# Kernel tuning notes

Measured on AMD Instinct MI355X. Metric: run time of the kernel, lower is better.

## Reference

```python
import jax, jax.numpy as jnp
import numpy as np
from functools import partial


def conv2d(x, w, b, pad):
    # x: [B,C,H,W], w: [O,I,kh,kw]
    out = jax.lax.conv_general_dilated(
        x, w, window_strides=(1, 1), padding=[(pad, pad), (pad, pad)],
        dimension_numbers=("NCHW", "OIHW", "NCHW"))
    return out + b[None, :, None, None]


def maxpool3x3_s1(x):
    return jax.lax.reduce_window(
        x, -jnp.inf, jax.lax.max, (1, 1, 3, 3), (1, 1, 1, 1),
        padding=((0, 0), (0, 0), (1, 1), (1, 1)))


def bilinear_sample(img, y, x):
    # img: [B,C,H,W]; y, x: [B,H,W] float sample coords. Zero outside bounds.
    def one(im, yy, xx):  # im [C,H,W]
        H, W = im.shape[1], im.shape[2]
        y0 = jnp.floor(yy)
        x0 = jnp.floor(xx)
        wy = yy - y0
        wx = xx - x0
        y0i = y0.astype(jnp.int32)
        x0i = x0.astype(jnp.int32)

        def g(yi, xi):
            valid = (yi >= 0) & (yi < H) & (xi >= 0) & (xi < W)
            yc = jnp.clip(yi, 0, H - 1)
            xc = jnp.clip(xi, 0, W - 1)
            return im[:, yc, xc] * valid[None].astype(im.dtype)

        return (g(y0i, x0i) * ((1 - wy) * (1 - wx))[None]
                + g(y0i, x0i + 1) * ((1 - wy) * wx)[None]
                + g(y0i + 1, x0i) * (wy * (1 - wx))[None]
                + g(y0i + 1, x0i + 1) * (wy * wx)[None])

    return jax.vmap(one)(img, y, x)


def deform_conv2d(x, offset, weight, bias, k, pad):
    # torchvision-style: offset [B, 2*k*k, H, W], pairs are (dy, dx) in
    # row-major kernel order. stride=1, dilation=1.
    B, C, H, W = x.shape
    off = offset.reshape(B, k * k, 2, H, W)
    hh = jnp.arange(H, dtype=x.dtype)[None, :, None]  # [1,H,1]
    ww = jnp.arange(W, dtype=x.dtype)[None, None, :]  # [1,1,W]
    out = jnp.zeros((B, weight.shape[0], H, W), x.dtype)
    for t in range(k * k):
        i, j = t // k, t % k
        y = hh + (i - pad) + off[:, t, 0]  # [B,H,W]
        xc = ww + (j - pad) + off[:, t, 1]
        s = bilinear_sample(x, y, xc)      # [B,C,H,W]
        out = out + jnp.einsum("bchw,oc->bohw", s, weight[:, :, i, j])
    return out + bias[None, :, None, None]


def _mk(key, shape, scale=0.05):
    return jax.random.normal(key, shape, dtype=jnp.float32) * scale


def setup_inputs() -> dict:
    key = jax.random.key(0)
    ks = jax.random.split(key, 20)
    C = 512
    Cb = C // 4  # 128
    B, H, W = 8, 64, 64
    return {
        "x": jax.random.normal(ks[0], (B, C, H, W), dtype=jnp.float32),
        "w_b1": _mk(ks[1], (Cb, C, 1, 1)), "b_b1": jnp.zeros((Cb,), jnp.float32),
        "w_b21": _mk(ks[2], (Cb, C, 1, 1)), "b_b21": jnp.zeros((Cb,), jnp.float32),
        "w_off2": _mk(ks[3], (18, Cb, 3, 3), 0.01), "b_off2": jnp.zeros((18,), jnp.float32),
        "w_ddc2": _mk(ks[4], (Cb, Cb, 3, 3)), "b_ddc2": jnp.zeros((Cb,), jnp.float32),
        "w_b31": _mk(ks[5], (Cb, C, 1, 1)), "b_b31": jnp.zeros((Cb,), jnp.float32),
        "w_off3": _mk(ks[6], (50, Cb, 5, 5), 0.01), "b_off3": jnp.zeros((50,), jnp.float32),
        "w_ddc3": _mk(ks[7], (Cb, Cb, 5, 5)), "b_ddc3": jnp.zeros((Cb,), jnp.float32),
        "w_b4": _mk(ks[8], (Cb, C, 1, 1)), "b_b4": jnp.zeros((Cb,), jnp.float32),
        "w_cc": _mk(ks[9], (C, Cb * 4, 1, 1)), "b_cc": jnp.zeros((C,), jnp.float32),
    }


def reference(x, w_b1, b_b1, w_b21, b_b21, w_off2, b_off2, w_ddc2, b_ddc2,
              w_b31, b_b31, w_off3, b_off3, w_ddc3, b_ddc3, w_b4, b_b4,
              w_cc, b_cc):
    b1 = conv2d(x, w_b1, b_b1, 0)

    b2i = conv2d(x, w_b21, b_b21, 0)
    off2 = conv2d(b2i, w_off2, b_off2, 1)
    b2 = deform_conv2d(b2i, off2, w_ddc2, b_ddc2, k=3, pad=1)

    b3i = conv2d(x, w_b31, b_b31, 0)
    off3 = conv2d(b3i, w_off3, b_off3, 2)
    b3 = deform_conv2d(b3i, off3, w_ddc3, b_ddc3, k=5, pad=2)

    b4 = conv2d(maxpool3x3_s1(x), w_b4, b_b4, 0)

    cat = jnp.concatenate([b1, b2, b3, b4], axis=1) * x
    fused = conv2d(cat, w_cc, b_cc, 0)
    return x + jax.nn.sigmoid(fused)
```

## Files before the change

### kernel.cpp

```cpp
#include <hip/hip_runtime.h>
#include <math.h>

#define HW 4096
typedef short short8 __attribute__((ext_vector_type(8)));
typedef float floatx4 __attribute__((ext_vector_type(4)));

#define O_XBT   0ull
#define O_PXB   33554432ull
#define O_CATB  67108864ull
#define O_WPB   100663296ull
#define O_W4B   101056512ull
#define O_WCCB  101187584ull
#define O_WD2T  101711872ull
#define O_WD3T  102006784ull
#define O_WO2T  102825984ull
#define O_WO3T  102973440ull
#define O_T2B   33554432ull
#define O_T3B   41943040ull
#define O_OFF2  50331648ull
#define O_OFF3  52690944ull

__device__ __forceinline__ unsigned short f2b(float f) {
    union { float f; unsigned u; } v; v.f = f;
    unsigned r = v.u + 0x7FFFu + ((v.u >> 16) & 1u);
    return (unsigned short)(r >> 16);
}
__device__ __forceinline__ float lou(unsigned u) {
    union { unsigned u; float f; } v; v.u = u << 16; return v.f;
}
__device__ __forceinline__ float hiu(unsigned u) {
    union { unsigned u; float f; } v; v.u = u & 0xFFFF0000u; return v.f;
}
__device__ __forceinline__ unsigned pk2(float lo, float hi) {
    return (unsigned)f2b(lo) | ((unsigned)f2b(hi) << 16);
}

__global__ __launch_bounds__(256) void k_prepw(
        const float* __restrict__ w1, const float* __restrict__ w21,
        const float* __restrict__ w31, const float* __restrict__ w4,
        const float* __restrict__ wcc, const float* __restrict__ wd2,
        const float* __restrict__ wd3, const float* __restrict__ wo2,
        const float* __restrict__ wo3, unsigned short* __restrict__ ws8) {
    unsigned i = blockIdx.x * 256 + threadIdx.x;
    unsigned short* wpb  = ws8 + (O_WPB  >> 1);
    unsigned short* w4b  = ws8 + (O_W4B  >> 1);
    unsigned short* wccb = ws8 + (O_WCCB >> 1);
    unsigned short* wd2t = ws8 + (O_WD2T >> 1);
    unsigned short* wd3t = ws8 + (O_WD3T >> 1);
    unsigned short* wo2t = ws8 + (O_WO2T >> 1);
    unsigned short* wo3t = ws8 + (O_WO3T >> 1);
    if (i < 196608) {
        int o = i >> 9;
        float v = (o < 128) ? w1[i] : (o < 256) ? w21[i - 65536] : w31[i - 131072];
        wpb[i] = f2b(v);
    } else if (i < 262144) {
        unsigned j = i - 196608; w4b[j] = f2b(w4[j]);
    } else if (i < 524288) {
        unsigned j = i - 262144; wccb[j] = f2b(wcc[j]);
    } else if (i < 671744) {
        unsigned j = i - 524288; int t = j >> 14, o = (j >> 7) & 127, c = j & 127;
        wd2t[j] = f2b(wd2[((o * 128 + c) * 9) + t]);
    } else if (i < 1081344) {
        unsigned j = i - 671744; int t = j >> 14, o = (j >> 7) & 127, c = j & 127;
        wd3t[j] = f2b(wd3[((o * 128 + c) * 25) + t]);
    } else if (i < 1155072) {
        unsigned j = i - 1081344; int t = j >> 13, o = (j >> 7) & 63, c = j & 127;
        wo2t[j] = (o < 18) ? f2b(wo2[((o * 128 + c) * 9) + t]) : 0;
    } else if (i < 1359872) {
        unsigned j = i - 1155072; int t = j >> 13, o = (j >> 7) & 63, c = j & 127;
        wo3t[j] = (o < 50) ? f2b(wo3[((o * 128 + c) * 25) + t]) : 0;
    }
}

__global__ __launch_bounds__(256) void k_xpose(const float* __restrict__ X,
                                               unsigned short* __restrict__ xbT) {
    __shared__ unsigned short t[32][33];
    const int p0 = blockIdx.x * 32, c0 = blockIdx.y * 32, b = blockIdx.z;
    const int tid = threadIdx.x;
    #pragma unroll
    for (int s = 0; s < 4; ++s) {
        int cl = s * 8 + (tid >> 5), pl = tid & 31;
        t[cl][pl] = f2b(X[((size_t)b * 512 + c0 + cl) * HW + p0 + pl]);
    }
    __syncthreads();
    #pragma unroll
    for (int s = 0; s < 4; ++s) {
        int pl = s * 8 + (tid >> 5), cl = tid & 31;
        xbT[((size_t)b * HW + p0 + pl) * 512 + c0 + cl] = t[cl][pl];
    }
}

__global__ __launch_bounds__(256) void k_pool(const unsigned short* __restrict__ xbT,
                                              unsigned short* __restrict__ pxb) {
    unsigned gid = blockIdx.x * 256 + threadIdx.x;
    int b = gid >> 18;
    unsigned rem = gid & 262143;
    int pos = rem >> 6;
    int cg = (rem & 63) * 8;
    int h = pos >> 6, w = pos & 63;
    const unsigned short* img = xbT + (size_t)b * HW * 512;
    float m[8] = {-INFINITY, -INFINITY, -INFINITY, -INFINITY,
                  -INFINITY, -INFINITY, -INFINITY, -INFINITY};
    #pragma unroll
    for (int dy = -1; dy <= 1; ++dy) {
        int hh = h + dy;
        if (hh < 0 || hh >= 64) continue;
        #pragma unroll
        for (int dx = -1; dx <= 1; ++dx) {
            int ww = w + dx;
            if (ww < 0 || ww >= 64) continue;
            uint4 v = *(const uint4*)(img + ((size_t)(hh * 64 + ww)) * 512 + cg);
            unsigned uu[4] = {v.x, v.y, v.z, v.w};
            #pragma unroll
            for (int e = 0; e < 4; ++e) {
                m[2 * e]     = fmaxf(m[2 * e],     lou(uu[e]));
                m[2 * e + 1] = fmaxf(m[2 * e + 1], hiu(uu[e]));
            }
        }
    }
    uint4 o;
    o.x = pk2(m[0], m[1]); o.y = pk2(m[2], m[3]);
    o.z = pk2(m[4], m[5]); o.w = pk2(m[6], m[7]);
    *(uint4*)(pxb + ((size_t)b * HW + pos) * 512 + cg) = o;
}

#define SA(r,c) SM[(r)*40 + (c)]
#define SB(r,c) SM[5120 + (r)*40 + (c)]
#define SC(r,c) SM[(r)*136 + (c)]
__global__ __launch_bounds__(256) void k_gemm(
        const unsigned short* __restrict__ A, const float* __restrict__ bias,
        const unsigned short* __restrict__ Bm,
        unsigned short* __restrict__ dst, int dStride, int dOff) {
    __shared__ unsigned short SM[17408];
    const int tid = threadIdx.x;
    const int n0 = blockIdx.x * 128;
    const int b = blockIdx.z;
    const int wave = tid >> 6, lane = tid & 63, quad = lane >> 4, lr = lane & 15;
    const int m0w = (wave & 1) * 64, n0w = (wave >> 1) * 64;
    const int srow = tid >> 1, skh = (tid & 1) * 16;
    floatx4 acc[4][4] = {};

    for (int k0 = 0; k0 < 512; k0 += 32) {
        const unsigned short* ga = A + (size_t)srow * 512 + k0 + skh;
        uint4 a0 = *(const uint4*)(ga);
        uint4 a1 = *(const uint4*)(ga + 8);
        const unsigned short* gb = Bm + ((size_t)b * HW + n0 + srow) * 512 + k0 + skh;
        uint4 b0 = *(const uint4*)(gb);
        uint4 b1 = *(const uint4*)(gb + 8);
        __syncthreads();
        *(uint4*)&SA(srow, skh) = a0;
        *(uint4*)&SA(srow, skh + 8) = a1;
        *(uint4*)&SB(srow, skh) = b0;
        *(uint4*)&SB(srow, skh + 8) = b1;
        __syncthreads();
        short8 af[4], bf[4];
        #pragma unroll
        for (int i = 0; i < 4; ++i) af[i] = *(short8*)&SA(m0w + i * 16 + lr, quad * 8);
        #pragma unroll
        for (int j = 0; j < 4; ++j) bf[j] = *(short8*)&SB(n0w + j * 16 + lr, quad * 8);
        #pragma unroll
        for (int i = 0; i < 4; ++i)
            #pragma unroll
            for (int j = 0; j < 4; ++j)
                acc[i][j] = __builtin_amdgcn_mfma_f32_16x16x32_bf16(af[i], bf[j], acc[i][j], 0, 0, 0);
    }
    __syncthreads();
    #pragma unroll
    for (int i = 0; i < 4; ++i) {
        float4 bs = *(const float4*)&bias[m0w + i * 16 + quad * 4];
        #pragma unroll
        for (int j = 0; j < 4; ++j) {
            floatx4 v = acc[i][j];
            int pos = n0w + j * 16 + lr;
            int ch = m0w + i * 16 + quad * 4;
            uint2 st;
            st.x = pk2(v[0] + bs.x, v[1] + bs.y);
            st.y = pk2(v[2] + bs.z, v[3] + bs.w);
            *(uint2*)&SC(pos, ch) = st;
        }
    }
    __syncthreads();
    #pragma unroll
    for (int r = 0; r < 8; ++r) {
        int pos = (tid >> 4) + r * 16;
        *(uint4*)&dst[((size_t)b * HW + n0 + pos) * dStride + dOff + (tid & 15) * 8] =
            *(uint4*)&SC(pos, (tid & 15) * 8);
    }
}

template<int KS, int OCH>
__global__ __launch_bounds__(512) void k_offconv2(
        const unsigned short* __restrict__ img,
        const unsigned short* __restrict__ woT,
        const float* __restrict__ bias, float* __restrict__ Out) {
    constexpr int PAD = KS / 2;
    constexpr int TT = KS * KS;
    constexpr int SR = 2 + 2 * PAD;
    constexpr int SC2 = 64 + 2 * PAD;
    constexpr int NE = SR * SC2;
    __shared__ unsigned short slab[NE * 36];
    __shared__ float ctile[64 * 132];
    const int tid = threadIdx.x;
    const int p0 = blockIdx.x * 128, hrow0 = blockIdx.x * 2, b = blockIdx.z;
    const int wave = tid >> 6, lane = tid & 63, quad = lane >> 4, lr = lane & 15;
    const int wm = wave & 1, wn = wave >> 1;
    const unsigned short* ib = img + (size_t)b * HW * 128;
    floatx4 acc[2][2] = {};

    for (int c0 = 0; c0 < 128; c0 += 32) {
        __syncthreads();
        if (tid < NE) {
            int s = tid / SC2, cl = tid % SC2;
            int r = hrow0 - PAD + s, cc = cl - PAD;
            uint4 v0 = {}, v1 = {}, v2 = {}, v3 = {};
            if ((unsigned)r < 64u && (unsigned)cc < 64u) {
                const uint4* g = (const uint4*)(ib + ((size_t)(r * 64 + cc)) * 128 + c0);
                v0 = g[0]; v1 = g[1]; v2 = g[2]; v3 = g[3];
            }
            uint2* d2 = (uint2*)&slab[tid * 36];
            d2[0] = make_uint2(v0.x, v0.y); d2[1] = make_uint2(v0.z, v0.w);
            d2[2] = make_uint2(v1.x, v1.y); d2[3] = make_uint2(v1.z, v1.w);
            d2[4] = make_uint2(v2.x, v2.y); d2[5] = make_uint2(v2.z, v2.w);
            d2[6] = make_uint2(v3.x, v3.y); d2[7] = make_uint2(v3.z, v3.w);
        }
        __syncthreads();
        #pragma unroll
        for (int t = 0; t < TT; ++t) {
            const int ky = t / KS, kx = t % KS;
            short8 af[2], bf[2];
            #pragma unroll
            for (int i = 0; i < 2; ++i)
                af[i] = *(const short8*)&woT[((size_t)t * 64 + wm * 32 + i * 16 + lr) * 128
                                             + c0 + quad * 8];
            #pragma unroll
            for (int j = 0; j < 2; ++j) {
                int p = wn * 32 + j * 16 + lr;
                int e = ((p >> 6) + ky) * SC2 + (p & 63) + kx;
                union { uint2 u[2]; short8 s; } bb;
                const uint2* sp = (const uint2*)&slab[e * 36 + quad * 8];
                bb.u[0] = sp[0]; bb.u[1] = sp[1];
                bf[j] = bb.s;
            }
            #pragma unroll
            for (int i = 0; i < 2; ++i)
                #pragma unroll
                for (int j = 0; j < 2; ++j)
                    acc[i][j] = __builtin_amdgcn_mfma_f32_16x16x32_bf16(af[i], bf[j], acc[i][j], 0, 0, 0);
        }
    }
    __syncthreads();
    #pragma unroll
    for (int i = 0; i < 2; ++i)
        #pragma unroll
        for (int j = 0; j < 2; ++j) {
            floatx4 v = acc[i][j];
            int p = wn * 32 + j * 16 + lr;
            int o = wm * 32 + i * 16 + quad * 4;
            #pragma unroll
            for (int rg = 0; rg < 4; ++rg)
                ctile[(o + rg) * 132 + p] = v[rg];
        }
    __syncthreads();
    {
        int o = tid >> 3, seg = tid & 7;
        if (o < OCH) {
            float bs = bias[o];
            const float* src = &ctile[o * 132 + seg * 16];
            float* dst = &Out[((size_t)b * OCH + o) * HW + p0 + seg * 16];
            #pragma unroll
            for (int q = 0; q < 4; ++q) {
                float4 v = *(const float4*)(src + q * 4);
                v.x += bs; v.y += bs; v.z += bs; v.w += bs;
                *(float4*)(dst + q * 4) = v;
            }
        }
    }
}

#define DC_GATHER(T, DY, DX) do {                                              \
    float fy = (float)(h + (T) / KS - PAD) + (DY);                             \
    float fx = (float)(w + (T) % KS - PAD) + (DX);                             \
    float y0f = floorf(fy), x0f = floorf(fx);                                  \
    float wyv = fy - y0f, wxv = fx - x0f;                                      \
    int y0 = (int)y0f, x0 = (int)x0f;                                          \
    w00 = (1.f - wyv) * (1.f - wxv); w01 = (1.f - wyv) * wxv;                  \
    w10 = wyv * (1.f - wxv);         w11 = wyv * wxv;                          \
    bool yv0 = (unsigned)y0 < 64u, yv1 = (unsigned)(y0 + 1) < 64u;             \
    bool xv0 = (unsigned)x0 < 64u, xv1 = (unsigned)(x0 + 1) < 64u;             \
    long bidx = (long)(y0 * 64 + x0) * 128 + cseg;                             \
    cn0 = z4; cn1 = z4; cn2 = z4; cn3 = z4;                                    \
    cn4 = z4; cn5 = z4; cn6 = z4; cn7 = z4;                                    \
    if (yv0 && xv0) { const uint4* p_ = (const uint4*)(ib + bidx);             \
        cn0 = p_[0]; cn1 = p_[1]; }                                            \
    if (yv0 && xv1) { const uint4* p_ = (const uint4*)(ib + bidx + 128);       \
        cn2 = p_[0]; cn3 = p_[1]; }                                            \
    if (yv1 && xv0) { const uint4* p_ = (const uint4*)(ib + bidx + 8192);      \
        cn4 = p_[0]; cn5 = p_[1]; }                                            \
    if (yv1 && xv1) { const uint4* p_ = (const uint4*)(ib + bidx + 8320);      \
        cn6 = p_[0]; cn7 = p_[1]; }                                            \
} while (0)

#define DC_BLEND(RA, RB, RC, RD, OUT) do {                                     \
    unsigned a_[4] = {RA.x, RA.y, RA.z, RA.w};                                 \
    unsigned b_[4] = {RB.x, RB.y, RB.z, RB.w};                                 \
    unsigned c_[4] = {RC.x, RC.y, RC.z, RC.w};                                 \
    unsigned d_[4] = {RD.x, RD.y, RD.z, RD.w};                                 \
    unsigned r_[4];                                                            \
    _Pragma("unroll")                                                          \
    for (int e_ = 0; e_ < 4; ++e_) {                                           \
        float lo_ = w00 * lou(a_[e_]) + w01 * lou(b_[e_])                      \
                  + w10 * lou(c_[e_]) + w11 * lou(d_[e_]);                     \
        float hi_ = w00 * hiu(a_[e_]) + w01 * hiu(b_[e_])                      \
                  + w10 * hiu(c_[e_]) + w11 * hiu(d_[e_]);                     \
        asm("v_cvt_pk_bf16_f32 %0, %1, %2"                                     \
            : "=v"(r_[e_]) : "v"(lo_), "v"(hi_));                              \
    }                                                                          \
    OUT.x = r_[0]; OUT.y = r_[1]; OUT.z = r_[2]; OUT.w = r_[3];                \
} while (0)

template<int KS>
__global__ __launch_bounds__(256, 4) void k_deform10(
        const unsigned short* __restrict__ img,
        const float* __restrict__ Off,
        const unsigned short* __restrict__ wdT,
        const float* __restrict__ bias,
        unsigned short* __restrict__ catb, int dOff) {
    constexpr int PAD = KS / 2;
    constexpr int TT = KS * KS;
    __shared__ unsigned short sS[2][32][136];
    const int tid = threadIdx.x;
    const int b = blockIdx.x & 7;
    const int tile = (blockIdx.x >> 3) + 16 * blockIdx.z;
    const int p0 = tile * 32;
    const int wave = tid >> 6, lane = tid & 63, quad = lane >> 4, lr = lane & 15;
    const int m0w = wave * 32;
    const int pos = tid >> 3;
    const int cseg = (tid & 7) * 16;
    const int pglob = p0 + pos;
    const int h = pglob >> 6, w = pglob & 63;
    const unsigned short* ib = img + (size_t)b * HW * 128;
    const float* offb = Off + (size_t)b * 2 * TT * HW;
    const uint4 z4 = make_uint4(0u, 0u, 0u, 0u);

    floatx4 acc00 = {}, acc01 = {}, acc10 = {}, acc11 = {};
    uint4 cn0, cn1, cn2, cn3, cn4, cn5, cn6, cn7;
    float w00, w01, w10, w11;
    float noy = 0.f, nox = 0.f;

    {
        float dy0 = offb[pglob];
        float dx0 = offb[HW + pglob];
        DC_GATHER(0, dy0, dx0);
    }
    if (TT > 1) { noy = offb[2 * HW + pglob]; nox = offb[3 * HW + pglob]; }

    for (int t = 0; t < TT; ++t) {
        const int cur = t & 1;
        uint4 ov0, ov1;
        DC_BLEND(cn0, cn2, cn4, cn6, ov0);
        DC_BLEND(cn1, cn3, cn5, cn7, ov1);
        *(uint4*)&sS[cur][pos][cseg] = ov0;
        *(uint4*)&sS[cur][pos][cseg + 8] = ov1;
        const unsigned short* wb = wdT + (size_t)t * 16384
                                   + (size_t)(m0w + lr) * 128 + quad * 8;
        short8 wr0 = *(const short8*)(wb);
        short8 wr1 = *(const short8*)(wb + 2048);
        short8 wr2 = *(const short8*)(wb + 32);
        short8 wr3 = *(const short8*)(wb + 2080);
        short8 wr4 = *(const short8*)(wb + 64);
        short8 wr5 = *(const short8*)(wb + 2112);
        short8 wr6 = *(const short8*)(wb + 96);
        short8 wr7 = *(const short8*)(wb + 2144);
        __syncthreads();
        if (t + 1 < TT) {
            DC_GATHER(t + 1, noy, nox);
            if (t + 2 < TT) {
                noy = offb[(size_t)(2 * t + 4) * HW + pglob];
                nox = offb[(size_t)(2 * t + 5) * HW + pglob];
            }
        }
        #pragma unroll
        for (int ks = 0; ks < 4; ++ks) {
            short8 bf0 = *(short8*)&sS[cur][lr][ks * 32 + quad * 8];
            short8 bf1 = *(short8*)&sS[cur][16 + lr][ks * 32 + quad * 8];
            short8 a0 = (ks == 0) ? wr0 : (ks == 1) ? wr2 : (ks == 2) ? wr4 : wr6;
            short8 a1 = (ks == 0) ? wr1 : (ks == 1) ? wr3 : (ks == 2) ? wr5 : wr7;
            acc00 = __builtin_amdgcn_mfma_f32_16x16x32_bf16(a0, bf0, acc00, 0, 0, 0);
            acc01 = __builtin_amdgcn_mfma_f32_16x16x32_bf16(a0, bf1, acc01, 0, 0, 0);
            acc10 = __builtin_amdgcn_mfma_f32_16x16x32_bf16(a1, bf0, acc10, 0, 0, 0);
            acc11 = __builtin_amdgcn_mfma_f32_16x16x32_bf16(a1, bf1, acc11, 0, 0, 0);
        }
    }
    __syncthreads();
    {
        float4 bs = *(const float4*)&bias[m0w + quad * 4];
        float4 bs2 = *(const float4*)&bias[m0w + 16 + quad * 4];
        floatx4 v;
        uint2 st;
        int ch0 = m0w + quad * 4, ch1 = m0w + 16 + quad * 4;
        v = acc00;
        st.x = pk2(v[0] + bs.x, v[1] + bs.y);
        st.y = pk2(v[2] + bs.z, v[3] + bs.w);
        *(uint2*)&sS[0][lr][ch0] = st;
        v = acc01;
        st.x = pk2(v[0] + bs.x, v[1] + bs.y);
        st.y = pk2(v[2] + bs.z, v[3] + bs.w);
        *(uint2*)&sS[0][16 + lr][ch0] = st;
        v = acc10;
        st.x = pk2(v[0] + bs2.x, v[1] + bs2.y);
        st.y = pk2(v[2] + bs2.z, v[3] + bs2.w);
        *(uint2*)&sS[0][lr][ch1] = st;
        v = acc11;
        st.x = pk2(v[0] + bs2.x, v[1] + bs2.y);
        st.y = pk2(v[2] + bs2.z, v[3] + bs2.w);
        *(uint2*)&sS[0][16 + lr][ch1] = st;
    }
    __syncthreads();
    #pragma unroll
    for (int r = 0; r < 2; ++r) {
        int idx = r * 256 + tid;
        int p = idx >> 4, sg = (idx & 15) * 8;
        *(uint4*)&catb[((size_t)b * HW + p0 + p) * 512 + dOff + sg] =
            *(uint4*)&sS[0][p][sg];
    }
}

__global__ __launch_bounds__(256) void k_gemm_final(
        const unsigned short* __restrict__ A, const float* __restrict__ bias,
        const unsigned short* __restrict__ catb, const unsigned short* __restrict__ xbT,
        const float* __restrict__ X, float* __restrict__ OutF) {
    __shared__ unsigned short sA[128][40];
    __shared__ unsigned short sB[128][40];
    const int tid = threadIdx.x;
    const int n0 = blockIdx.x * 128;
    const int o0 = blockIdx.y * 128;
    const int b = blockIdx.z;
    const int wave = tid >> 6, lane = tid & 63, quad = lane >> 4, lr = lane & 15;
    const int m0w = (wave & 1) * 64, n0w = (wave >> 1) * 64;
    const int srow = tid >> 1, skh = (tid & 1) * 16;
    floatx4 acc[4][4] = {};

    for (int k0 = 0; k0 < 512; k0 += 32) {
        const unsigned short* ga = A + (size_t)(o0 + srow) * 512 + k0 + skh;
        uint4 a0 = *(const uint4*)(ga);
        uint4 a1 = *(const uint4*)(ga + 8);
        size_t bi = ((size_t)b * HW + n0 + srow) * 512 + k0 + skh;
        uint4 c0 = *(const uint4*)(catb + bi);
        uint4 c1 = *(const uint4*)(catb + bi + 8);
        uint4 x0 = *(const uint4*)(xbT + bi);
        uint4 x1 = *(const uint4*)(xbT + bi + 8);
        unsigned cu[8] = {c0.x, c0.y, c0.z, c0.w, c1.x, c1.y, c1.z, c1.w};
        unsigned xu[8] = {x0.x, x0.y, x0.z, x0.w, x1.x, x1.y, x1.z, x1.w};
        unsigned mu[8];
        #pragma unroll
        for (int e = 0; e < 8; ++e)
            mu[e] = pk2(lou(cu[e]) * lou(xu[e]), hiu(cu[e]) * hiu(xu[e]));
        __syncthreads();
        *(uint4*)&sA[srow][skh] = a0;
        *(uint4*)&sA[srow][skh + 8] = a1;
        uint4 m0v; m0v.x = mu[0]; m0v.y = mu[1]; m0v.z = mu[2]; m0v.w = mu[3];
        uint4 m1v; m1v.x = mu[4]; m1v.y = mu[5]; m1v.z = mu[6]; m1v.w = mu[7];
        *(uint4*)&sB[srow][skh] = m0v;
        *(uint4*)&sB[srow][skh + 8] = m1v;
        __syncthreads();
        short8 af[4], bf[4];
        #pragma unroll
        for (int i = 0; i < 4; ++i) af[i] = *(short8*)&sA[m0w + i * 16 + lr][quad * 8];
        #pragma unroll
        for (int j = 0; j < 4; ++j) bf[j] = *(short8*)&sB[n0w + j * 16 + lr][quad * 8];
        #pragma unroll
        for (int i = 0; i < 4; ++i)
            #pragma unroll
            for (int j = 0; j < 4; ++j)
                acc[i][j] = __builtin_amdgcn_mfma_f32_16x16x32_bf16(af[i], bf[j], acc[i][j], 0, 0, 0);
    }
    #pragma unroll
    for (int i = 0; i < 4; ++i) {
        float4 bs = *(const float4*)&bias[o0 + m0w + i * 16 + quad * 4];
        float bsa[4] = {bs.x, bs.y, bs.z, bs.w};
        #pragma unroll
        for (int j = 0; j < 4; ++j) {
            floatx4 v = acc[i][j];
            int pos = n0 + n0w + j * 16 + lr;
            #pragma unroll
            for (int rg = 0; rg < 4; ++rg) {
                int o = o0 + m0w + i * 16 + quad * 4 + rg;
                float f = v[rg] + bsa[rg];
                float sg = 1.f / (1.f + __expf(-f));
                size_t idx = ((size_t)b * 512 + o) * HW + pos;
                OutF[idx] = X[idx] + sg;
            }
        }
    }
}

extern "C" void kernel_launch(void* const* d_in, const int* in_sizes, int n_in,
                              void* d_out, int out_size, void* d_ws, size_t ws_size,
                              hipStream_t stream) {
    const float* x      = (const float*)d_in[0];
    const float* w_b1   = (const float*)d_in[1];
    const float* b_b1   = (const float*)d_in[2];
    const float* w_b21  = (const float*)d_in[3];
    const float* b_b21  = (const float*)d_in[4];
    const float* w_off2 = (const float*)d_in[5];
    const float* b_off2 = (const float*)d_in[6];
    const float* w_ddc2 = (const float*)d_in[7];
    const float* b_ddc2 = (const float*)d_in[8];
    const float* w_b31  = (const float*)d_in[9];
    const float* b_b31  = (const float*)d_in[10];
    const float* w_off3 = (const float*)d_in[11];
    const float* b_off3 = (const float*)d_in[12];
    const float* w_ddc3 = (const float*)d_in[13];
    const float* b_ddc3 = (const float*)d_in[14];
    const float* w_b4   = (const float*)d_in[15];
    const float* b_b4   = (const float*)d_in[16];
    const float* w_cc   = (const float*)d_in[17];
    const float* b_cc   = (const float*)d_in[18];

    char* wsb = (char*)d_ws;
    unsigned short* ws8  = (unsigned short*)d_ws;
    unsigned short* xbT  = (unsigned short*)(wsb + O_XBT);
    unsigned short* pxb  = (unsigned short*)(wsb + O_PXB);
    unsigned short* catb = (unsigned short*)(wsb + O_CATB);
    unsigned short* wpb  = (unsigned short*)(wsb + O_WPB);
    unsigned short* w4b  = (unsigned short*)(wsb + O_W4B);
    unsigned short* wccb = (unsigned short*)(wsb + O_WCCB);
    unsigned short* wd2t = (unsigned short*)(wsb + O_WD2T);
    unsigned short* wd3t = (unsigned short*)(wsb + O_WD3T);
    unsigned short* wo2t = (unsigned short*)(wsb + O_WO2T);
    unsigned short* wo3t = (unsigned short*)(wsb + O_WO3T);
    unsigned short* t2b  = (unsigned short*)(wsb + O_T2B);
    unsigned short* t3b  = (unsigned short*)(wsb + O_T3B);
    float* off2 = (float*)(wsb + O_OFF2);
    float* off3 = (float*)(wsb + O_OFF3);
    float* out  = (float*)d_out;

    k_prepw<<<dim3(5312), dim3(256), 0, stream>>>(
        w_b1, w_b21, w_b31, w_b4, w_cc, w_ddc2, w_ddc3, w_off2, w_off3, ws8);
    k_xpose<<<dim3(128, 16, 8), dim3(256), 0, stream>>>(x, xbT);
    k_pool<<<dim3(8192), dim3(256), 0, stream>>>(xbT, pxb);
    k_gemm<<<dim3(32, 1, 8), dim3(256), 0, stream>>>(w4b, b_b4, pxb, catb, 512, 384);
    k_gemm<<<dim3(32, 1, 8), dim3(256), 0, stream>>>(wpb, b_b1, xbT, catb, 512, 0);
    k_gemm<<<dim3(32, 1, 8), dim3(256), 0, stream>>>(wpb + 128 * 512, b_b21, xbT, t2b, 128, 0);
    k_gemm<<<dim3(32, 1, 8), dim3(256), 0, stream>>>(wpb + 256 * 512, b_b31, xbT, t3b, 128, 0);
    k_offconv2<3, 18><<<dim3(32, 1, 8), dim3(512), 0, stream>>>(t2b, wo2t, b_off2, off2);
    k_offconv2<5, 50><<<dim3(32, 1, 8), dim3(512), 0, stream>>>(t3b, wo3t, b_off3, off3);
    k_deform10<3><<<dim3(128, 1, 8), dim3(256), 0, stream>>>(t2b, off2, wd2t, b_ddc2, catb, 128);
    k_deform10<5><<<dim3(128, 1, 8), dim3(256), 0, stream>>>(t3b, off3, wd3t, b_ddc3, catb, 256);
    k_gemm_final<<<dim3(32, 4, 8), dim3(256), 0, stream>>>(wccb, b_cc, catb, xbT, x, out);
}
```

Before: 545.7 us.

## Batch deform-conv taps into groups of KS with double-buffered gathers

The deformable conv kernel now gathers and blends KS kernel taps into a KS-deep shared-memory buffer, then runs all MFMAs for the group after a single barrier. This replaces the per-tap double buffer, which needed one barrier per tap. Register double-buffering (A/B sets) keeps the next gather in flight during blending, and s_setprio raises wave priority during the MFMA phase. In exchange it uses more shared memory and registers, and the occupancy hint drops from 4 to 3 blocks per CU.

```diff
diff --git a/kernel.cpp b/kernel.cpp
--- a/kernel.cpp
+++ b/kernel.cpp
@@ -277,7 +277,7 @@
     }
 }
 
-#define DC_GATHER(T, DY, DX) do {                                              \
+#define DCG(S, T, DY, DX) do {                                                 \
     float fy = (float)(h + (T) / KS - PAD) + (DY);                             \
     float fx = (float)(w + (T) % KS - PAD) + (DX);                             \
     float y0f = floorf(fy), x0f = floorf(fx);                                  \
@@ -288,26 +288,30 @@
     bool yv0 = (unsigned)y0 < 64u, yv1 = (unsigned)(y0 + 1) < 64u;             \
     bool xv0 = (unsigned)x0 < 64u, xv1 = (unsigned)(x0 + 1) < 64u;             \
     long bidx = (long)(y0 * 64 + x0) * 128 + cseg;                             \
-    cn0 = z4; cn1 = z4; cn2 = z4; cn3 = z4;                                    \
-    cn4 = z4; cn5 = z4; cn6 = z4; cn7 = z4;                                    \
+    cn##S##0 = z4; cn##S##1 = z4; cn##S##2 = z4; cn##S##3 = z4;                \
+    cn##S##4 = z4; cn##S##5 = z4; cn##S##6 = z4; cn##S##7 = z4;                \
     if (yv0 && xv0) { const uint4* p_ = (const uint4*)(ib + bidx);             \
-        cn0 = p_[0]; cn1 = p_[1]; }                                            \
+        cn##S##0 = p_[0]; cn##S##1 = p_[1]; }                                  \
     if (yv0 && xv1) { const uint4* p_ = (const uint4*)(ib + bidx + 128);       \
-        cn2 = p_[0]; cn3 = p_[1]; }                                            \
+        cn##S##2 = p_[0]; cn##S##3 = p_[1]; }                                  \
     if (yv1 && xv0) { const uint4* p_ = (const uint4*)(ib + bidx + 8192);      \
-        cn4 = p_[0]; cn5 = p_[1]; }                                            \
+        cn##S##4 = p_[0]; cn##S##5 = p_[1]; }                                  \
     if (yv1 && xv1) { const uint4* p_ = (const uint4*)(ib + bidx + 8320);      \
-        cn6 = p_[0]; cn7 = p_[1]; }                                            \
+        cn##S##6 = p_[0]; cn##S##7 = p_[1]; }                                  \
 } while (0)
 
-#define DC_BLEND(RA, RB, RC, RD, OUT) do {                                     \
-    unsigned a_[4] = {RA.x, RA.y, RA.z, RA.w};                                 \
-    unsigned b_[4] = {RB.x, RB.y, RB.z, RB.w};                                 \
-    unsigned c_[4] = {RC.x, RC.y, RC.z, RC.w};                                 \
-    unsigned d_[4] = {RD.x, RD.y, RD.z, RD.w};                                 \
-    unsigned r_[4];                                                            \
+#define DCB(S, O0, O1) do {                                                    \
+    unsigned a_[8] = {(cn##S##0).x, (cn##S##0).y, (cn##S##0).z, (cn##S##0).w,  \
+                      (cn##S##1).x, (cn##S##1).y, (cn##S##1).z, (cn##S##1).w}; \
+    unsigned b_[8] = {(cn##S##2).x, (cn##S##2).y, (cn##S##2).z, (cn##S##2).w,  \
+                      (cn##S##3).x, (cn##S##3).y, (cn##S##3).z, (cn##S##3).w}; \
+    unsigned c_[8] = {(cn##S##4).x, (cn##S##4).y, (cn##S##4).z, (cn##S##4).w,  \
+                      (cn##S##5).x, (cn##S##5).y, (cn##S##5).z, (cn##S##5).w}; \
+    unsigned d_[8] = {(cn##S##6).x, (cn##S##6).y, (cn##S##6).z, (cn##S##6).w,  \
+                      (cn##S##7).x, (cn##S##7).y, (cn##S##7).z, (cn##S##7).w}; \
+    unsigned r_[8];                                                            \
     _Pragma("unroll")                                                          \
-    for (int e_ = 0; e_ < 4; ++e_) {                                           \
+    for (int e_ = 0; e_ < 8; ++e_) {                                           \
         float lo_ = w00 * lou(a_[e_]) + w01 * lou(b_[e_])                      \
                   + w10 * lou(c_[e_]) + w11 * lou(d_[e_]);                     \
         float hi_ = w00 * hiu(a_[e_]) + w01 * hiu(b_[e_])                      \
@@ -315,11 +319,12 @@
         asm("v_cvt_pk_bf16_f32 %0, %1, %2"                                     \
             : "=v"(r_[e_]) : "v"(lo_), "v"(hi_));                              \
     }                                                                          \
-    OUT.x = r_[0]; OUT.y = r_[1]; OUT.z = r_[2]; OUT.w = r_[3];                \
+    O0.x = r_[0]; O0.y = r_[1]; O0.z = r_[2]; O0.w = r_[3];                    \
+    O1.x = r_[4]; O1.y = r_[5]; O1.z = r_[6]; O1.w = r_[7];                    \
 } while (0)
 
 template<int KS>
-__global__ __launch_bounds__(256, 4) void k_deform10(
+__global__ __launch_bounds__(256, 3) void k_deform11(
         const unsigned short* __restrict__ img,
         const float* __restrict__ Off,
         const unsigned short* __restrict__ wdT,
@@ -327,7 +332,9 @@
         unsigned short* __restrict__ catb, int dOff) {
     constexpr int PAD = KS / 2;
     constexpr int TT = KS * KS;
-    __shared__ unsigned short sS[2][32][136];
+    constexpr int GS = KS;
+    constexpr int NG = KS;
+    __shared__ unsigned short sS[GS][32][136];
     const int tid = threadIdx.x;
     const int b = blockIdx.x & 7;
     const int tile = (blockIdx.x >> 3) + 16 * blockIdx.z;
@@ -343,55 +350,75 @@
     const uint4 z4 = make_uint4(0u, 0u, 0u, 0u);
 
     floatx4 acc00 = {}, acc01 = {}, acc10 = {}, acc11 = {};
-    uint4 cn0, cn1, cn2, cn3, cn4, cn5, cn6, cn7;
+    uint4 cnA0, cnA1, cnA2, cnA3, cnA4, cnA5, cnA6, cnA7;
+    uint4 cnB0, cnB1, cnB2, cnB3, cnB4, cnB5, cnB6, cnB7;
     float w00, w01, w10, w11;
-    float noy = 0.f, nox = 0.f;
+    float noy, nox;
 
     {
         float dy0 = offb[pglob];
         float dx0 = offb[HW + pglob];
-        DC_GATHER(0, dy0, dx0);
-    }
-    if (TT > 1) { noy = offb[2 * HW + pglob]; nox = offb[3 * HW + pglob]; }
-
-    for (int t = 0; t < TT; ++t) {
-        const int cur = t & 1;
-        uint4 ov0, ov1;
-        DC_BLEND(cn0, cn2, cn4, cn6, ov0);
-        DC_BLEND(cn1, cn3, cn5, cn7, ov1);
-        *(uint4*)&sS[cur][pos][cseg] = ov0;
-        *(uint4*)&sS[cur][pos][cseg + 8] = ov1;
-        const unsigned short* wb = wdT + (size_t)t * 16384
-                                   + (size_t)(m0w + lr) * 128 + quad * 8;
-        short8 wr0 = *(const short8*)(wb);
-        short8 wr1 = *(const short8*)(wb + 2048);
-        short8 wr2 = *(const short8*)(wb + 32);
-        short8 wr3 = *(const short8*)(wb + 2080);
-        short8 wr4 = *(const short8*)(wb + 64);
-        short8 wr5 = *(const short8*)(wb + 2112);
-        short8 wr6 = *(const short8*)(wb + 96);
-        short8 wr7 = *(const short8*)(wb + 2144);
-        __syncthreads();
-        if (t + 1 < TT) {
-            DC_GATHER(t + 1, noy, nox);
-            if (t + 2 < TT) {
-                noy = offb[(size_t)(2 * t + 4) * HW + pglob];
-                nox = offb[(size_t)(2 * t + 5) * HW + pglob];
-            }
-        }
-        #pragma unroll
-        for (int ks = 0; ks < 4; ++ks) {
-            short8 bf0 = *(short8*)&sS[cur][lr][ks * 32 + quad * 8];
-            short8 bf1 = *(short8*)&sS[cur][16 + lr][ks * 32 + quad * 8];
-            short8 a0 = (ks == 0) ? wr0 : (ks == 1) ? wr2 : (ks == 2) ? wr4 : wr6;
-            short8 a1 = (ks == 0) ? wr1 : (ks == 1) ? wr3 : (ks == 2) ? wr5 : wr7;
-            acc00 = __builtin_amdgcn_mfma_f32_16x16x32_bf16(a0, bf0, acc00, 0, 0, 0);
-            acc01 = __builtin_amdgcn_mfma_f32_16x16x32_bf16(a0, bf1, acc01, 0, 0, 0);
-            acc10 = __builtin_amdgcn_mfma_f32_16x16x32_bf16(a1, bf0, acc10, 0, 0, 0);
-            acc11 = __builtin_amdgcn_mfma_f32_16x16x32_bf16(a1, bf1, acc11, 0, 0, 0);
-        }
-    }
-    __syncthreads();
+        DCG(A, 0, dy0, dx0);
+    }
+    noy = offb[2 * HW + pglob];
+    nox = offb[3 * HW + pglob];
+
+    for (int g = 0; g < NG; ++g) {
+        const int t0 = g * GS;
+        #pragma unroll
+        for (int tt = 0; tt < GS; ++tt) {
+            uint4 ov0, ov1;
+            if ((tt & 1) == 0) { DCB(A, ov0, ov1); } else { DCB(B, ov0, ov1); }
+            *(uint4*)&sS[tt][pos][cseg] = ov0;
+            *(uint4*)&sS[tt][pos][cseg + 8] = ov1;
+            if (tt < GS - 1) {
+                const int tn = t0 + tt + 1;
+                if ((tt & 1) == 0) { DCG(B, tn, noy, nox); }
+                else               { DCG(A, tn, noy, nox); }
+                if (tn + 1 < TT) {
+                    noy = offb[(size_t)(2 * tn + 2) * HW + pglob];
+                    nox = offb[(size_t)(2 * tn + 3) * HW + pglob];
+                }
+            }
+        }
+        __syncthreads();
+        if (g + 1 < NG) {
+            const int tn = t0 + GS;
+            DCG(A, tn, noy, nox);
+            if (tn + 1 < TT) {
+                noy = offb[(size_t)(2 * tn + 2) * HW + pglob];
+                nox = offb[(size_t)(2 * tn + 3) * HW + pglob];
+            }
+        }
+        __builtin_amdgcn_s_setprio(1);
+        #pragma unroll
+        for (int tt = 0; tt < GS; ++tt) {
+            const int t = t0 + tt;
+            const unsigned short* wb = wdT + (size_t)t * 16384
+                                       + (size_t)(m0w + lr) * 128 + quad * 8;
+            short8 wr0 = *(const short8*)(wb);
+            short8 wr1 = *(const short8*)(wb + 2048);
+            short8 wr2 = *(const short8*)(wb + 32);
+            short8 wr3 = *(const short8*)(wb + 2080);
+            short8 wr4 = *(const short8*)(wb + 64);
+            short8 wr5 = *(const short8*)(wb + 2112);
+            short8 wr6 = *(const short8*)(wb + 96);
+            short8 wr7 = *(const short8*)(wb + 2144);
+            #pragma unroll
+            for (int ks = 0; ks < 4; ++ks) {
+                short8 bf0 = *(short8*)&sS[tt][lr][ks * 32 + quad * 8];
+                short8 bf1 = *(short8*)&sS[tt][16 + lr][ks * 32 + quad * 8];
+                short8 a0 = (ks == 0) ? wr0 : (ks == 1) ? wr2 : (ks == 2) ? wr4 : wr6;
+                short8 a1 = (ks == 0) ? wr1 : (ks == 1) ? wr3 : (ks == 2) ? wr5 : wr7;
+                acc00 = __builtin_amdgcn_mfma_f32_16x16x32_bf16(a0, bf0, acc00, 0, 0, 0);
+                acc01 = __builtin_amdgcn_mfma_f32_16x16x32_bf16(a0, bf1, acc01, 0, 0, 0);
+                acc10 = __builtin_amdgcn_mfma_f32_16x16x32_bf16(a1, bf0, acc10, 0, 0, 0);
+                acc11 = __builtin_amdgcn_mfma_f32_16x16x32_bf16(a1, bf1, acc11, 0, 0, 0);
+            }
+        }
+        __builtin_amdgcn_s_setprio(0);
+        __syncthreads();
+    }
     {
         float4 bs = *(const float4*)&bias[m0w + quad * 4];
         float4 bs2 = *(const float4*)&bias[m0w + 16 + quad * 4];
@@ -545,7 +572,7 @@
     k_gemm<<<dim3(32, 1, 8), dim3(256), 0, stream>>>(wpb + 256 * 512, b_b31, xbT, t3b, 128, 0);
     k_offconv2<3, 18><<<dim3(32, 1, 8), dim3(512), 0, stream>>>(t2b, wo2t, b_off2, off2);
     k_offconv2<5, 50><<<dim3(32, 1, 8), dim3(512), 0, stream>>>(t3b, wo3t, b_off3, off3);
-    k_deform10<3><<<dim3(128, 1, 8), dim3(256), 0, stream>>>(t2b, off2, wd2t, b_ddc2, catb, 128);
-    k_deform10<5><<<dim3(128, 1, 8), dim3(256), 0, stream>>>(t3b, off3, wd3t, b_ddc3, catb, 256);
+    k_deform11<3><<<dim3(128, 1, 8), dim3(256), 0, stream>>>(t2b, off2, wd2t, b_ddc2, catb, 128);
+    k_deform11<5><<<dim3(128, 1, 8), dim3(256), 0, stream>>>(t3b, off3, wd3t, b_ddc3, catb, 256);
     k_gemm_final<<<dim3(32, 4, 8), dim3(256), 0, stream>>>(wccb, b_cc, catb, xbT, x, out);
 }
```

Result: no change. 548.6 us (+0.5%).
